# Kernel tuning notes

Measured on AMD Instinct MI355X. Metric: run time of the kernel, lower is better.

## Reference

```python
import jax, jax.numpy as jnp
import numpy as np

N_NODES = 100_000
N_EDGES = 3_200_000
F_IN = 64
HID = 16
N_CLASSES = 4


def setup_inputs() -> dict:
    key = jax.random.key(0)
    ks = jax.random.split(key, 9)
    x = jax.random.normal(ks[0], (N_NODES, F_IN), dtype=jnp.float32)
    edge_index = jax.random.randint(ks[1], (2, N_EDGES), 0, N_NODES, dtype=jnp.int64)
    edge_weight = jax.random.uniform(ks[2], (N_EDGES,), dtype=jnp.float32)
    # Glorot-style init for the three GCN layer weights, zero bias (PyG default)
    W1 = jax.random.normal(ks[3], (F_IN, HID), dtype=jnp.float32) * (1.0 / np.sqrt(F_IN))
    b1 = jnp.zeros((HID,), jnp.float32)
    W3 = jax.random.normal(ks[4], (HID, HID), dtype=jnp.float32) * (1.0 / np.sqrt(HID))
    b3 = jnp.zeros((HID,), jnp.float32)
    W2 = jax.random.normal(ks[5], (HID, N_CLASSES), dtype=jnp.float32) * (1.0 / np.sqrt(HID))
    b2 = jnp.zeros((N_CLASSES,), jnp.float32)
    return {"x": x, "edge_index": edge_index, "edge_weight": edge_weight,
            "W1": W1, "b1": b1, "W3": W3, "b3": b3, "W2": W2, "b2": b2}


def reference(x, edge_index, edge_weight, W1, b1, W3, b3, W2, b2):
    n = x.shape[0]
    # GCNConv default: add self-loops with weight 1, symmetric deg^-1/2 norm
    loop = jnp.arange(n, dtype=edge_index.dtype)
    row = jnp.concatenate([edge_index[0], loop])  # source nodes
    col = jnp.concatenate([edge_index[1], loop])  # target nodes
    ew = jnp.concatenate([edge_weight, jnp.ones((n,), edge_weight.dtype)])
    deg = jax.ops.segment_sum(ew, col, num_segments=n)
    dinv = jnp.where(deg > 0, jax.lax.rsqrt(deg), 0.0)
    norm = dinv[row] * ew * dinv[col]  # [E+N]

    def gcn_conv(h, W, b):
        h = h @ W                                  # [N, out] small matmul first
        msg = norm[:, None] * h[row]               # gather + scale, [E+N, out]
        return jax.ops.segment_sum(msg, col, num_segments=n) + b

    h = jax.nn.relu(gcn_conv(x, W1, b1))
    # dropout is identity in eval mode (training=False)
    h = jax.nn.relu(gcn_conv(h, W3, b3))
    h = gcn_conv(h, W2, b2)
    return jax.nn.log_softmax(h, axis=1)
```

## Files before the change

kernel.cpp:

```cpp
#include <hip/hip_runtime.h>
#include <math.h>

#define NN 100000
#define NE 3200000
#define F_IN 64
#define HID 16
#define NC 4

#define SZB 200
#define NB 500
#define CAP 7424
#define CH 8192
#define NCH 391
#define NW 16

typedef _Float16 half_t;
typedef _Float16 h4f __attribute__((ext_vector_type(4)));

__device__ __forceinline__ unsigned bdiv(unsigned c) {
    return (unsigned)(((unsigned long long)c * 167773ull) >> 25);
}

__device__ __forceinline__ float upw(int pk) {
    unsigned short us = (unsigned short)(pk & 0x7fff);
    half_t h;
    __builtin_memcpy(&h, &us, 2);
    return (float)h;
}

__global__ __launch_bounds__(1024) void k_bin(const int* __restrict__ row,
                                              const int* __restrict__ col,
                                              const float* __restrict__ ew,
                                              int* __restrict__ cursor,
                                              unsigned* __restrict__ bpk,
                                              unsigned char* __restrict__ bcl) {
    __shared__ int h[NB];
    __shared__ int lstart[NB];
    __shared__ int gbase[NB];
    __shared__ int wsum[8];
    __shared__ unsigned spk[CH];
    __shared__ unsigned short sbk[CH];
    __shared__ unsigned char scl[CH];
    int tid = threadIdx.x;
    int lane = tid & 63, wv = tid >> 6;
    for (int i = tid; i < NB; i += 1024) h[i] = 0;
    __syncthreads();
    int e0 = blockIdx.x * CH;
    int e1 = min(e0 + CH, NE);
    int eCnt = e1 - e0;
    for (int i = e0 + tid * 4; i < e1; i += 1024 * 4) {
        int4 c4 = *(const int4*)(col + i);
        atomicAdd(&h[bdiv(c4.x)], 1);
        atomicAdd(&h[bdiv(c4.y)], 1);
        atomicAdd(&h[bdiv(c4.z)], 1);
        atomicAdd(&h[bdiv(c4.w)], 1);
    }
    __syncthreads();
    int c0 = (tid < NB) ? h[tid] : 0;
    int v = c0;
#pragma unroll
    for (int off = 1; off < 64; off <<= 1) {
        int t = __shfl_up(v, off, 64);
        if (lane >= off) v += t;
    }
    if (wv < 8 && lane == 63) wsum[wv] = v;
    __syncthreads();
    if (tid < NB) {
        int pre = 0;
#pragma unroll
        for (int ww = 0; ww < 8; ww++) pre += (ww < wv) ? wsum[ww] : 0;
        int ex = (v + pre) - c0;
        lstart[tid] = ex;
        h[tid] = ex;
        if (c0) gbase[tid] = tid * CAP + atomicAdd(&cursor[tid], c0);
    }
    __syncthreads();
    for (int i = e0 + tid * 4; i < e1; i += 1024 * 4) {
        int4 c4 = *(const int4*)(col + i);
        int4 r4 = *(const int4*)(row + i);
        float4 w4 = *(const float4*)(ew + i);
        half_t hw0 = (half_t)w4.x, hw1 = (half_t)w4.y, hw2 = (half_t)w4.z, hw3 = (half_t)w4.w;
        unsigned short b0, b1, b2, b3;
        __builtin_memcpy(&b0, &hw0, 2); __builtin_memcpy(&b1, &hw1, 2);
        __builtin_memcpy(&b2, &hw2, 2); __builtin_memcpy(&b3, &hw3, 2);
        int p; unsigned bb;
        bb = bdiv(c4.x); p = atomicAdd(&h[bb], 1);
        spk[p] = ((unsigned)r4.x << 15) | (b0 & 0x7fff); scl[p] = (unsigned char)(c4.x - 200u * bb);
        sbk[p] = (unsigned short)bb;
        bb = bdiv(c4.y); p = atomicAdd(&h[bb], 1);
        spk[p] = ((unsigned)r4.y << 15) | (b1 & 0x7fff); scl[p] = (unsigned char)(c4.y - 200u * bb);
        sbk[p] = (unsigned short)bb;
        bb = bdiv(c4.z); p = atomicAdd(&h[bb], 1);
        spk[p] = ((unsigned)r4.z << 15) | (b2 & 0x7fff); scl[p] = (unsigned char)(c4.z - 200u * bb);
        sbk[p] = (unsigned short)bb;
        bb = bdiv(c4.w); p = atomicAdd(&h[bb], 1);
        spk[p] = ((unsigned)r4.w << 15) | (b3 & 0x7fff); scl[p] = (unsigned char)(c4.w - 200u * bb);
        sbk[p] = (unsigned short)bb;
    }
    __syncthreads();
    for (int i = tid; i < eCnt; i += 1024) {
        int lo = sbk[i];
        int d = gbase[lo] + (i - lstart[lo]);
        if (d < (lo + 1) * CAP) {
            bpk[d] = spk[i];
            bcl[d] = scl[i];
        }
    }
}

__global__ __launch_bounds__(1024) void k_sort(const unsigned* __restrict__ bpk,
                                               const unsigned char* __restrict__ bcl,
                                               const int* __restrict__ cursor,
                                               const float* __restrict__ x,
                                               const float* __restrict__ W1,
                                               unsigned* __restrict__ epk,
                                               int2* __restrict__ nodeptr2,
                                               float* __restrict__ dinv,
                                               half_t* __restrict__ tt1) {
    __shared__ int hw[NW][SZB];
    __shared__ int cnt[SZB];
    __shared__ int ps[SZB];
    __shared__ int wsum4[4];
    __shared__ unsigned stage[CAP];
    __shared__ float Ws[F_IN * HID];
    int b = blockIdx.x, tid = threadIdx.x;
    int lane = tid & 63;
    int w = tid >> 6;
    for (int i = tid; i < NW * SZB; i += 1024) ((int*)hw)[i] = 0;
    for (int i = tid; i < F_IN * HID; i += 1024) Ws[i] = W1[i];
    __syncthreads();
    int s = b * CAP;
    int m = min(cursor[b], CAP);
    int e = s + m;
    for (int i = s + tid; i < e; i += 1024)
        atomicAdd(&hw[w][bcl[i]], 1);
    __syncthreads();
    if (tid < SZB) {
        int c = 0;
#pragma unroll
        for (int ww = 0; ww < NW; ww++) c += hw[ww][tid];
        cnt[tid] = c;
    }
    __syncthreads();
    int pc = (tid < SZB) ? ((cnt[tid] + 3) & ~3) : 0;
    int v = pc;
#pragma unroll
    for (int off = 1; off < 64; off <<= 1) {
        int t = __shfl_up(v, off, 64);
        if (lane >= off) v += t;
    }
    if (w < 4 && lane == 63) wsum4[w] = v;
    __syncthreads();
    if (tid < SZB) {
        int pre = 0;
#pragma unroll
        for (int ww = 0; ww < 4; ww++) pre += (ww < w) ? wsum4[ww] : 0;
        ps[tid] = v + pre;
    }
    __syncthreads();
    if (tid < SZB) {
        int run = ps[tid] - pc;
#pragma unroll
        for (int ww = 0; ww < NW; ww++) {
            int t = hw[ww][tid];
            hw[ww][tid] = run;
            run += t;
        }
    }
    __syncthreads();
    int mpad = min(ps[SZB - 1], CAP);
    for (int i = tid; i < mpad; i += 1024) stage[i] = 0u;
    __syncthreads();
    for (int i = s + tid; i < e; i += 1024) {
        int cl = bcl[i];
        int pos = atomicAdd(&hw[w][cl], 1);
        if (pos < CAP) stage[pos] = bpk[i];
    }
    __syncthreads();
    for (int i = tid; i < mpad; i += 1024) epk[s + i] = stage[i];
    int nl = tid >> 2, l = tid & 3;
    float di = 0.0f;
    int n = b * SZB + nl;
    if (nl < SZB) {
        int pcn = (cnt[nl] + 3) & ~3;
        int ex = ps[nl] - pcn;
        float sw = 0.0f;
        for (int i = ex + l; i < ex + pcn; i += 4) sw += upw((int)stage[i]);
        sw += __shfl_xor(sw, 1, 4);
        sw += __shfl_xor(sw, 2, 4);
        di = rsqrtf(1.0f + sw);
        if (n < NN && l == 0) {
            nodeptr2[n] = make_int2(s + ex, s + ex + pcn);
            dinv[n] = di;
        }
    }
    if (nl < SZB && n < NN) {
        float part[HID];
#pragma unroll
        for (int j = 0; j < HID; j++) part[j] = 0.0f;
        const float4* xp = (const float4*)(x + (size_t)n * F_IN) + l * 4;
#pragma unroll
        for (int k4 = 0; k4 < 4; k4++) {
            float4 vx = xp[k4];
            int k = l * 16 + k4 * 4;
#pragma unroll
            for (int j = 0; j < HID; j++) {
                part[j] += vx.x * Ws[(k + 0) * HID + j];
                part[j] += vx.y * Ws[(k + 1) * HID + j];
                part[j] += vx.z * Ws[(k + 2) * HID + j];
                part[j] += vx.w * Ws[(k + 3) * HID + j];
            }
        }
#pragma unroll
        for (int j = 0; j < HID; j++) {
            part[j] += __shfl_xor(part[j], 1, 4);
            part[j] += __shfl_xor(part[j], 2, 4);
        }
        h4f o;
        o.x = (half_t)(di * part[4 * l + 0]);
        o.y = (half_t)(di * part[4 * l + 1]);
        o.z = (half_t)(di * part[4 * l + 2]);
        o.w = (half_t)(di * part[4 * l + 3]);
        ((h4f*)tt1)[n * 4 + l] = o;
    }
}

#define ACC4(Q, V0, V1, V2, V3)                                                 \
    do {                                                                        \
        float w0 = upw((Q).x), w1 = upw((Q).y), w2 = upw((Q).z), w3 = upw((Q).w); \
        ax += w0 * (float)(V0).x; ay += w0 * (float)(V0).y;                     \
        az += w0 * (float)(V0).z; aw += w0 * (float)(V0).w;                     \
        ax += w1 * (float)(V1).x; ay += w1 * (float)(V1).y;                     \
        az += w1 * (float)(V1).z; aw += w1 * (float)(V1).w;                     \
        ax += w2 * (float)(V2).x; ay += w2 * (float)(V2).y;                     \
        az += w2 * (float)(V2).z; aw += w2 * (float)(V2).w;                     \
        ax += w3 * (float)(V3).x; ay += w3 * (float)(V3).y;                     \
        az += w3 * (float)(V3).z; aw += w3 * (float)(V3).w;                     \
    } while (0)

template <int DN>
__global__ __launch_bounds__(256) void k_aggf(const unsigned* __restrict__ epk,
                                              const int2* __restrict__ nptr,
                                              const half_t* __restrict__ tt_in,
                                              const float* __restrict__ bias,
                                              const float* __restrict__ dinv,
                                              const float* __restrict__ Wn,
                                              half_t* __restrict__ tt_out) {
    __shared__ float Ws[HID * DN];
    if (threadIdx.x < HID * DN) Ws[threadIdx.x] = Wn[threadIdx.x];
    __syncthreads();
    int tid = blockIdx.x * 256 + threadIdx.x;
    int n = tid >> 2;
    int l = tid & 3;
    if (n >= NN) return;
    int2 p = nptr[n];
    const h4f* ttp = (const h4f*)tt_in;
    h4f sv = ttp[n * 4 + l];
    float ax = 0.f, ay = 0.f, az = 0.f, aw = 0.f;
    int base = p.x;
    const int pend = p.y;
    if (base < pend) {
        int4 q = *(const int4*)(epk + base);
        base += 4;
        bool more = base < pend;
        int4 qn = *(const int4*)(epk + (more ? base : p.x));
        h4f v0 = ttp[((((unsigned)q.x) >> 15) << 2) + l];
        h4f v1 = ttp[((((unsigned)q.y) >> 15) << 2) + l];
        h4f v2 = ttp[((((unsigned)q.z) >> 15) << 2) + l];
        h4f v3 = ttp[((((unsigned)q.w) >> 15) << 2) + l];
        while (more) {
            base += 4;
            bool more2 = base < pend;
            int4 qnn = *(const int4*)(epk + (more2 ? base : p.x));
            h4f u0 = ttp[((((unsigned)qn.x) >> 15) << 2) + l];
            h4f u1 = ttp[((((unsigned)qn.y) >> 15) << 2) + l];
            h4f u2 = ttp[((((unsigned)qn.z) >> 15) << 2) + l];
            h4f u3 = ttp[((((unsigned)qn.w) >> 15) << 2) + l];
            ACC4(q, v0, v1, v2, v3);
            q = qn; qn = qnn;
            v0 = u0; v1 = u1; v2 = u2; v3 = u3;
            more = more2;
        }
        ACC4(q, v0, v1, v2, v3);
    }
    float di = dinv[n];
    const float4* b4p = (const float4*)bias;
    float4 b4 = b4p[l];
    float hreg[4];
    hreg[0] = fmaxf(b4.x + di * (ax + (float)sv.x), 0.f);
    hreg[1] = fmaxf(b4.y + di * (ay + (float)sv.y), 0.f);
    hreg[2] = fmaxf(b4.z + di * (az + (float)sv.z), 0.f);
    hreg[3] = fmaxf(b4.w + di * (aw + (float)sv.w), 0.f);
    if (DN == 16) {
        float ox = 0.f, oy = 0.f, oz = 0.f, ow = 0.f;
#pragma unroll
        for (int k = 0; k < HID; k++) {
            float hk = __shfl(hreg[k & 3], k >> 2, 4);
            const float4 wk = *(const float4*)&Ws[k * 16 + 4 * l];
            ox += hk * wk.x; oy += hk * wk.y; oz += hk * wk.z; ow += hk * wk.w;
        }
        h4f ov;
        ov.x = (half_t)(di * ox); ov.y = (half_t)(di * oy);
        ov.z = (half_t)(di * oz); ov.w = (half_t)(di * ow);
        ((h4f*)tt_out)[n * 4 + l] = ov;
    } else {
        float o = 0.f;
#pragma unroll
        for (int k = 0; k < HID; k++) {
            float hk = __shfl(hreg[k & 3], k >> 2, 4);
            o += hk * Ws[k * DN + l];
        }
        tt_out[(size_t)n * DN + l] = (half_t)(di * o);
    }
}

__global__ __launch_bounds__(256) void k_agg4sm(const unsigned* __restrict__ epk,
                                                const int2* __restrict__ nptr,
                                                const half_t* __restrict__ tt,
                                                const float* __restrict__ bias,
                                                const float* __restrict__ dinv,
                                                float* __restrict__ out) {
    int tid = blockIdx.x * 256 + threadIdx.x;
    int n = tid >> 2;
    int l = tid & 3;
    if (n >= NN) return;
    int2 p = nptr[n];
    float self = (float)tt[n * 4 + l];
    float acc = 0.f;
    int base = p.x;
    const int pend = p.y;
    if (base < pend) {
        int4 q = *(const int4*)(epk + base);
        base += 4;
        bool more = base < pend;
        int4 qn = *(const int4*)(epk + (more ? base : p.x));
        float v0 = (float)tt[((((unsigned)q.x) >> 15) << 2) + l];
        float v1 = (float)tt[((((unsigned)q.y) >> 15) << 2) + l];
        float v2 = (float)tt[((((unsigned)q.z) >> 15) << 2) + l];
        float v3 = (float)tt[((((unsigned)q.w) >> 15) << 2) + l];
        while (more) {
            base += 4;
            bool more2 = base < pend;
            int4 qnn = *(const int4*)(epk + (more2 ? base : p.x));
            float u0 = (float)tt[((((unsigned)qn.x) >> 15) << 2) + l];
            float u1 = (float)tt[((((unsigned)qn.y) >> 15) << 2) + l];
            float u2 = (float)tt[((((unsigned)qn.z) >> 15) << 2) + l];
            float u3 = (float)tt[((((unsigned)qn.w) >> 15) << 2) + l];
            acc += upw(q.x) * v0;
            acc += upw(q.y) * v1;
            acc += upw(q.z) * v2;
            acc += upw(q.w) * v3;
            q = qn; qn = qnn;
            v0 = u0; v1 = u1; v2 = u2; v3 = u3;
            more = more2;
        }
        acc += upw(q.x) * v0;
        acc += upw(q.y) * v1;
        acc += upw(q.z) * v2;
        acc += upw(q.w) * v3;
    }
    float di = dinv[n];
    float logit = bias[l] + di * (acc + self);
    float mx = logit;
    mx = fmaxf(mx, __shfl_xor(mx, 1, 4));
    mx = fmaxf(mx, __shfl_xor(mx, 2, 4));
    float ex = expf(logit - mx);
    float sm = ex;
    sm += __shfl_xor(sm, 1, 4);
    sm += __shfl_xor(sm, 2, 4);
    out[n * 4 + l] = logit - mx - logf(sm);
}

extern "C" void kernel_launch(void* const* d_in, const int* in_sizes, int n_in,
                              void* d_out, int out_size, void* d_ws, size_t ws_size,
                              hipStream_t stream) {
    const float* x  = (const float*)d_in[0];
    const int*   ei = (const int*)d_in[1];
    const float* ew = (const float*)d_in[2];
    const float* W1 = (const float*)d_in[3];
    const float* b1 = (const float*)d_in[4];
    const float* W3 = (const float*)d_in[5];
    const float* b3 = (const float*)d_in[6];
    const float* W2 = (const float*)d_in[7];
    const float* b2 = (const float*)d_in[8];
    float* out = (float*)d_out;

    const int* row = ei;
    const int* col = ei + NE;

    const size_t NEP = (size_t)NB * CAP;
    char* ws = (char*)d_ws;
    size_t off = 0;
    float*         dinv     = (float*)(ws + off);         off += 400000;
    int2*          nodeptr2 = (int2*)(ws + off);          off += 800000;
    int*           cursor   = (int*)(ws + off);           off += 2048;
    unsigned*      epk      = (unsigned*)(ws + off);      off += NEP * 4;
    unsigned*      bpk      = (unsigned*)(ws + off);      off += NEP * 4;
    unsigned char* bcl      = (unsigned char*)(ws + off); off += (NEP + 15) & ~15ull;
    half_t*        tt1      = (half_t*)(ws + off);        off += (size_t)NN * HID * 2;
    half_t*        tt2      = (half_t*)(ws + off);        off += (size_t)NN * HID * 2;
    half_t*        tt3      = (half_t*)(ws + off);        off += (size_t)NN * NC * 2;

    hipMemsetAsync(cursor, 0, NB * sizeof(int), stream);

    k_bin<<<NCH, 1024, 0, stream>>>(row, col, ew, cursor, bpk, bcl);
    k_sort<<<NB, 1024, 0, stream>>>(bpk, bcl, cursor, x, W1, epk, nodeptr2, dinv, tt1);

    int gA = (NN * 4 + 255) / 256;

    k_aggf<HID><<<gA, 256, 0, stream>>>(epk, nodeptr2, tt1, b1, dinv, W3, tt2);
    k_aggf<NC><<<gA, 256, 0, stream>>>(epk, nodeptr2, tt2, b3, dinv, W2, tt3);
    k_agg4sm<<<gA, 256, 0, stream>>>(epk, nodeptr2, tt3, b2, dinv, out);
}
```

Before: 220.9 us.

## Use nontemporal loads/stores for streaming data and halve bin chunk size

Streaming reads and writes of edge lists, node pointers, features and outputs are switched to nontemporal loads and stores, so they pollute the cache less and leave room for the randomly gathered feature tables. The binning kernel now processes chunks of 4096 edges with 512-thread blocks, giving twice as many blocks with less shared memory each. The risk is that nontemporal hints hurt data that is reused soon, such as bpk/bcl, which are read again by the next kernel, and epk, which is re-read by all three aggregation passes.

```diff
diff --git a/kernel.cpp b/kernel.cpp
--- a/kernel.cpp
+++ b/kernel.cpp
@@ -10,12 +10,15 @@
 #define SZB 200
 #define NB 500
 #define CAP 7424
-#define CH 8192
-#define NCH 391
+#define CH 4096
+#define NCH 782
 #define NW 16
 
 typedef _Float16 half_t;
 typedef _Float16 h4f __attribute__((ext_vector_type(4)));
+typedef int i4v __attribute__((ext_vector_type(4)));
+typedef int i2v __attribute__((ext_vector_type(2)));
+typedef float f4v __attribute__((ext_vector_type(4)));
 
 __device__ __forceinline__ unsigned bdiv(unsigned c) {
     return (unsigned)(((unsigned long long)c * 167773ull) >> 25);
@@ -28,12 +31,12 @@
     return (float)h;
 }
 
-__global__ __launch_bounds__(1024) void k_bin(const int* __restrict__ row,
-                                              const int* __restrict__ col,
-                                              const float* __restrict__ ew,
-                                              int* __restrict__ cursor,
-                                              unsigned* __restrict__ bpk,
-                                              unsigned char* __restrict__ bcl) {
+__global__ __launch_bounds__(512) void k_bin(const int* __restrict__ row,
+                                             const int* __restrict__ col,
+                                             const float* __restrict__ ew,
+                                             int* __restrict__ cursor,
+                                             unsigned* __restrict__ bpk,
+                                             unsigned char* __restrict__ bcl) {
     __shared__ int h[NB];
     __shared__ int lstart[NB];
     __shared__ int gbase[NB];
@@ -43,12 +46,12 @@
     __shared__ unsigned char scl[CH];
     int tid = threadIdx.x;
     int lane = tid & 63, wv = tid >> 6;
-    for (int i = tid; i < NB; i += 1024) h[i] = 0;
+    for (int i = tid; i < NB; i += 512) h[i] = 0;
     __syncthreads();
     int e0 = blockIdx.x * CH;
     int e1 = min(e0 + CH, NE);
     int eCnt = e1 - e0;
-    for (int i = e0 + tid * 4; i < e1; i += 1024 * 4) {
+    for (int i = e0 + tid * 4; i < e1; i += 512 * 4) {
         int4 c4 = *(const int4*)(col + i);
         atomicAdd(&h[bdiv(c4.x)], 1);
         atomicAdd(&h[bdiv(c4.y)], 1);
@@ -63,7 +66,7 @@
         int t = __shfl_up(v, off, 64);
         if (lane >= off) v += t;
     }
-    if (wv < 8 && lane == 63) wsum[wv] = v;
+    if (lane == 63) wsum[wv] = v;
     __syncthreads();
     if (tid < NB) {
         int pre = 0;
@@ -75,10 +78,10 @@
         if (c0) gbase[tid] = tid * CAP + atomicAdd(&cursor[tid], c0);
     }
     __syncthreads();
-    for (int i = e0 + tid * 4; i < e1; i += 1024 * 4) {
+    for (int i = e0 + tid * 4; i < e1; i += 512 * 4) {
         int4 c4 = *(const int4*)(col + i);
-        int4 r4 = *(const int4*)(row + i);
-        float4 w4 = *(const float4*)(ew + i);
+        i4v r4 = __builtin_nontemporal_load((const i4v*)(row + i));
+        f4v w4 = __builtin_nontemporal_load((const f4v*)(ew + i));
         half_t hw0 = (half_t)w4.x, hw1 = (half_t)w4.y, hw2 = (half_t)w4.z, hw3 = (half_t)w4.w;
         unsigned short b0, b1, b2, b3;
         __builtin_memcpy(&b0, &hw0, 2); __builtin_memcpy(&b1, &hw1, 2);
@@ -98,12 +101,12 @@
         sbk[p] = (unsigned short)bb;
     }
     __syncthreads();
-    for (int i = tid; i < eCnt; i += 1024) {
+    for (int i = tid; i < eCnt; i += 512) {
         int lo = sbk[i];
         int d = gbase[lo] + (i - lstart[lo]);
         if (d < (lo + 1) * CAP) {
-            bpk[d] = spk[i];
-            bcl[d] = scl[i];
+            __builtin_nontemporal_store(spk[i], bpk + d);
+            __builtin_nontemporal_store(scl[i], bcl + d);
         }
     }
 }
@@ -172,12 +175,14 @@
     for (int i = tid; i < mpad; i += 1024) stage[i] = 0u;
     __syncthreads();
     for (int i = s + tid; i < e; i += 1024) {
-        int cl = bcl[i];
+        int cl = __builtin_nontemporal_load(bcl + i);
         int pos = atomicAdd(&hw[w][cl], 1);
-        if (pos < CAP) stage[pos] = bpk[i];
-    }
-    __syncthreads();
-    for (int i = tid; i < mpad; i += 1024) epk[s + i] = stage[i];
+        unsigned pk = __builtin_nontemporal_load(bpk + i);
+        if (pos < CAP) stage[pos] = pk;
+    }
+    __syncthreads();
+    for (int i = tid; i < mpad; i += 1024)
+        __builtin_nontemporal_store(stage[i], epk + s + i);
     int nl = tid >> 2, l = tid & 3;
     float di = 0.0f;
     int n = b * SZB + nl;
@@ -198,10 +203,10 @@
         float part[HID];
 #pragma unroll
         for (int j = 0; j < HID; j++) part[j] = 0.0f;
-        const float4* xp = (const float4*)(x + (size_t)n * F_IN) + l * 4;
+        const f4v* xp = (const f4v*)(x + (size_t)n * F_IN) + l * 4;
 #pragma unroll
         for (int k4 = 0; k4 < 4; k4++) {
-            float4 vx = xp[k4];
+            f4v vx = __builtin_nontemporal_load(xp + k4);
             int k = l * 16 + k4 * 4;
 #pragma unroll
             for (int j = 0; j < HID; j++) {
@@ -221,7 +226,7 @@
         o.y = (half_t)(di * part[4 * l + 1]);
         o.z = (half_t)(di * part[4 * l + 2]);
         o.w = (half_t)(di * part[4 * l + 3]);
-        ((h4f*)tt1)[n * 4 + l] = o;
+        __builtin_nontemporal_store(o, ((h4f*)tt1) + n * 4 + l);
     }
 }
 
@@ -253,17 +258,17 @@
     int n = tid >> 2;
     int l = tid & 3;
     if (n >= NN) return;
-    int2 p = nptr[n];
+    i2v p = __builtin_nontemporal_load((const i2v*)nptr + n);
     const h4f* ttp = (const h4f*)tt_in;
     h4f sv = ttp[n * 4 + l];
     float ax = 0.f, ay = 0.f, az = 0.f, aw = 0.f;
     int base = p.x;
     const int pend = p.y;
     if (base < pend) {
-        int4 q = *(const int4*)(epk + base);
+        i4v q = __builtin_nontemporal_load((const i4v*)(epk + base));
         base += 4;
         bool more = base < pend;
-        int4 qn = *(const int4*)(epk + (more ? base : p.x));
+        i4v qn = __builtin_nontemporal_load((const i4v*)(epk + (more ? base : p.x)));
         h4f v0 = ttp[((((unsigned)q.x) >> 15) << 2) + l];
         h4f v1 = ttp[((((unsigned)q.y) >> 15) << 2) + l];
         h4f v2 = ttp[((((unsigned)q.z) >> 15) << 2) + l];
@@ -271,7 +276,7 @@
         while (more) {
             base += 4;
             bool more2 = base < pend;
-            int4 qnn = *(const int4*)(epk + (more2 ? base : p.x));
+            i4v qnn = __builtin_nontemporal_load((const i4v*)(epk + (more2 ? base : p.x)));
             h4f u0 = ttp[((((unsigned)qn.x) >> 15) << 2) + l];
             h4f u1 = ttp[((((unsigned)qn.y) >> 15) << 2) + l];
             h4f u2 = ttp[((((unsigned)qn.z) >> 15) << 2) + l];
@@ -283,7 +288,7 @@
         }
         ACC4(q, v0, v1, v2, v3);
     }
-    float di = dinv[n];
+    float di = __builtin_nontemporal_load(dinv + n);
     const float4* b4p = (const float4*)bias;
     float4 b4 = b4p[l];
     float hreg[4];
@@ -302,7 +307,7 @@
         h4f ov;
         ov.x = (half_t)(di * ox); ov.y = (half_t)(di * oy);
         ov.z = (half_t)(di * oz); ov.w = (half_t)(di * ow);
-        ((h4f*)tt_out)[n * 4 + l] = ov;
+        __builtin_nontemporal_store(ov, ((h4f*)tt_out) + n * 4 + l);
     } else {
         float o = 0.f;
 #pragma unroll
@@ -310,7 +315,7 @@
             float hk = __shfl(hreg[k & 3], k >> 2, 4);
             o += hk * Ws[k * DN + l];
         }
-        tt_out[(size_t)n * DN + l] = (half_t)(di * o);
+        __builtin_nontemporal_store((half_t)(di * o), tt_out + (size_t)n * DN + l);
     }
 }
 
@@ -324,16 +329,16 @@
     int n = tid >> 2;
     int l = tid & 3;
     if (n >= NN) return;
-    int2 p = nptr[n];
+    i2v p = __builtin_nontemporal_load((const i2v*)nptr + n);
     float self = (float)tt[n * 4 + l];
     float acc = 0.f;
     int base = p.x;
     const int pend = p.y;
     if (base < pend) {
-        int4 q = *(const int4*)(epk + base);
+        i4v q = __builtin_nontemporal_load((const i4v*)(epk + base));
         base += 4;
         bool more = base < pend;
-        int4 qn = *(const int4*)(epk + (more ? base : p.x));
+        i4v qn = __builtin_nontemporal_load((const i4v*)(epk + (more ? base : p.x)));
         float v0 = (float)tt[((((unsigned)q.x) >> 15) << 2) + l];
         float v1 = (float)tt[((((unsigned)q.y) >> 15) << 2) + l];
         float v2 = (float)tt[((((unsigned)q.z) >> 15) << 2) + l];
@@ -341,7 +346,7 @@
         while (more) {
             base += 4;
             bool more2 = base < pend;
-            int4 qnn = *(const int4*)(epk + (more2 ? base : p.x));
+            i4v qnn = __builtin_nontemporal_load((const i4v*)(epk + (more2 ? base : p.x)));
             float u0 = (float)tt[((((unsigned)qn.x) >> 15) << 2) + l];
             float u1 = (float)tt[((((unsigned)qn.y) >> 15) << 2) + l];
             float u2 = (float)tt[((((unsigned)qn.z) >> 15) << 2) + l];
@@ -359,7 +364,7 @@
         acc += upw(q.z) * v2;
         acc += upw(q.w) * v3;
     }
-    float di = dinv[n];
+    float di = __builtin_nontemporal_load(dinv + n);
     float logit = bias[l] + di * (acc + self);
     float mx = logit;
     mx = fmaxf(mx, __shfl_xor(mx, 1, 4));
@@ -368,7 +373,7 @@
     float sm = ex;
     sm += __shfl_xor(sm, 1, 4);
     sm += __shfl_xor(sm, 2, 4);
-    out[n * 4 + l] = logit - mx - logf(sm);
+    __builtin_nontemporal_store(logit - mx - logf(sm), out + n * 4 + l);
 }
 
 extern "C" void kernel_launch(void* const* d_in, const int* in_sizes, int n_in,
@@ -403,7 +408,7 @@
 
     hipMemsetAsync(cursor, 0, NB * sizeof(int), stream);
 
-    k_bin<<<NCH, 1024, 0, stream>>>(row, col, ew, cursor, bpk, bcl);
+    k_bin<<<NCH, 512, 0, stream>>>(row, col, ew, cursor, bpk, bcl);
     k_sort<<<NB, 1024, 0, stream>>>(bpk, bcl, cursor, x, W1, epk, nodeptr2, dinv, tt1);
 
     int gA = (NN * 4 + 255) / 256;
```

Result: slower. 299.5 us (+35.5%).

## Degree-sort nodes per bucket for balanced aggregation; pack bin staging into uint2

Applied to the files above, without the earlier changes.

In k_sort, each bucket's 200 nodes are counting-sorted by padded degree into a perm array. The three aggregation kernels then index nodes through perm, so lanes within a wavefront get similar edge counts and lose less time to divergence. k_bin now packs its shared staging into one uint2 per edge and keeps the col loads in registers instead of reading them twice. This adds an indirection load per node, scatters the output writes, and extra work in k_sort.

```diff
diff --git a/kernel.cpp b/kernel.cpp
--- a/kernel.cpp
+++ b/kernel.cpp
@@ -37,10 +37,8 @@
     __shared__ int h[NB];
     __shared__ int lstart[NB];
     __shared__ int gbase[NB];
-    __shared__ int wsum[8];
-    __shared__ unsigned spk[CH];
-    __shared__ unsigned short sbk[CH];
-    __shared__ unsigned char scl[CH];
+    __shared__ int wsum[16];
+    __shared__ uint2 s2[CH];
     int tid = threadIdx.x;
     int lane = tid & 63, wv = tid >> 6;
     for (int i = tid; i < NB; i += 1024) h[i] = 0;
@@ -48,12 +46,18 @@
     int e0 = blockIdx.x * CH;
     int e1 = min(e0 + CH, NE);
     int eCnt = e1 - e0;
-    for (int i = e0 + tid * 4; i < e1; i += 1024 * 4) {
-        int4 c4 = *(const int4*)(col + i);
-        atomicAdd(&h[bdiv(c4.x)], 1);
-        atomicAdd(&h[bdiv(c4.y)], 1);
-        atomicAdd(&h[bdiv(c4.z)], 1);
-        atomicAdd(&h[bdiv(c4.w)], 1);
+    int4 c4s[2];
+#pragma unroll
+    for (int it = 0; it < 2; it++) {
+        int i = e0 + tid * 4 + it * 4096;
+        if (i < e1) {
+            int4 c4 = *(const int4*)(col + i);
+            c4s[it] = c4;
+            atomicAdd(&h[bdiv(c4.x)], 1);
+            atomicAdd(&h[bdiv(c4.y)], 1);
+            atomicAdd(&h[bdiv(c4.z)], 1);
+            atomicAdd(&h[bdiv(c4.w)], 1);
+        }
     }
     __syncthreads();
     int c0 = (tid < NB) ? h[tid] : 0;
@@ -63,7 +67,7 @@
         int t = __shfl_up(v, off, 64);
         if (lane >= off) v += t;
     }
-    if (wv < 8 && lane == 63) wsum[wv] = v;
+    if (lane == 63) wsum[wv] = v;
     __syncthreads();
     if (tid < NB) {
         int pre = 0;
@@ -75,35 +79,40 @@
         if (c0) gbase[tid] = tid * CAP + atomicAdd(&cursor[tid], c0);
     }
     __syncthreads();
-    for (int i = e0 + tid * 4; i < e1; i += 1024 * 4) {
-        int4 c4 = *(const int4*)(col + i);
-        int4 r4 = *(const int4*)(row + i);
-        float4 w4 = *(const float4*)(ew + i);
-        half_t hw0 = (half_t)w4.x, hw1 = (half_t)w4.y, hw2 = (half_t)w4.z, hw3 = (half_t)w4.w;
-        unsigned short b0, b1, b2, b3;
-        __builtin_memcpy(&b0, &hw0, 2); __builtin_memcpy(&b1, &hw1, 2);
-        __builtin_memcpy(&b2, &hw2, 2); __builtin_memcpy(&b3, &hw3, 2);
-        int p; unsigned bb;
-        bb = bdiv(c4.x); p = atomicAdd(&h[bb], 1);
-        spk[p] = ((unsigned)r4.x << 15) | (b0 & 0x7fff); scl[p] = (unsigned char)(c4.x - 200u * bb);
-        sbk[p] = (unsigned short)bb;
-        bb = bdiv(c4.y); p = atomicAdd(&h[bb], 1);
-        spk[p] = ((unsigned)r4.y << 15) | (b1 & 0x7fff); scl[p] = (unsigned char)(c4.y - 200u * bb);
-        sbk[p] = (unsigned short)bb;
-        bb = bdiv(c4.z); p = atomicAdd(&h[bb], 1);
-        spk[p] = ((unsigned)r4.z << 15) | (b2 & 0x7fff); scl[p] = (unsigned char)(c4.z - 200u * bb);
-        sbk[p] = (unsigned short)bb;
-        bb = bdiv(c4.w); p = atomicAdd(&h[bb], 1);
-        spk[p] = ((unsigned)r4.w << 15) | (b3 & 0x7fff); scl[p] = (unsigned char)(c4.w - 200u * bb);
-        sbk[p] = (unsigned short)bb;
+#pragma unroll
+    for (int it = 0; it < 2; it++) {
+        int i = e0 + tid * 4 + it * 4096;
+        if (i < e1) {
+            int4 c4 = c4s[it];
+            int4 r4 = *(const int4*)(row + i);
+            float4 w4 = *(const float4*)(ew + i);
+            half_t hw0 = (half_t)w4.x, hw1 = (half_t)w4.y, hw2 = (half_t)w4.z, hw3 = (half_t)w4.w;
+            unsigned short b0, b1, b2, b3;
+            __builtin_memcpy(&b0, &hw0, 2); __builtin_memcpy(&b1, &hw1, 2);
+            __builtin_memcpy(&b2, &hw2, 2); __builtin_memcpy(&b3, &hw3, 2);
+            int p; unsigned bb;
+            bb = bdiv(c4.x); p = atomicAdd(&h[bb], 1);
+            s2[p] = make_uint2(((unsigned)r4.x << 15) | (b0 & 0x7fff),
+                               (bb << 8) | (unsigned)(c4.x - 200u * bb));
+            bb = bdiv(c4.y); p = atomicAdd(&h[bb], 1);
+            s2[p] = make_uint2(((unsigned)r4.y << 15) | (b1 & 0x7fff),
+                               (bb << 8) | (unsigned)(c4.y - 200u * bb));
+            bb = bdiv(c4.z); p = atomicAdd(&h[bb], 1);
+            s2[p] = make_uint2(((unsigned)r4.z << 15) | (b2 & 0x7fff),
+                               (bb << 8) | (unsigned)(c4.z - 200u * bb));
+            bb = bdiv(c4.w); p = atomicAdd(&h[bb], 1);
+            s2[p] = make_uint2(((unsigned)r4.w << 15) | (b3 & 0x7fff),
+                               (bb << 8) | (unsigned)(c4.w - 200u * bb));
+        }
     }
     __syncthreads();
     for (int i = tid; i < eCnt; i += 1024) {
-        int lo = sbk[i];
+        uint2 e2 = s2[i];
+        int lo = (int)(e2.y >> 8);
         int d = gbase[lo] + (i - lstart[lo]);
         if (d < (lo + 1) * CAP) {
-            bpk[d] = spk[i];
-            bcl[d] = scl[i];
+            bpk[d] = e2.x;
+            bcl[d] = (unsigned char)(e2.y & 255u);
         }
     }
 }
@@ -116,11 +125,14 @@
                                                unsigned* __restrict__ epk,
                                                int2* __restrict__ nodeptr2,
                                                float* __restrict__ dinv,
-                                               half_t* __restrict__ tt1) {
+                                               half_t* __restrict__ tt1,
+                                               int* __restrict__ perm) {
     __shared__ int hw[NW][SZB];
     __shared__ int cnt[SZB];
     __shared__ int ps[SZB];
     __shared__ int wsum4[4];
+    __shared__ int h2[64];
+    __shared__ int h2b[64];
     __shared__ unsigned stage[CAP];
     __shared__ float Ws[F_IN * HID];
     int b = blockIdx.x, tid = threadIdx.x;
@@ -128,6 +140,7 @@
     int w = tid >> 6;
     for (int i = tid; i < NW * SZB; i += 1024) ((int*)hw)[i] = 0;
     for (int i = tid; i < F_IN * HID; i += 1024) Ws[i] = W1[i];
+    if (tid < 64) h2[tid] = 0;
     __syncthreads();
     int s = b * CAP;
     int m = min(cursor[b], CAP);
@@ -143,6 +156,11 @@
     }
     __syncthreads();
     int pc = (tid < SZB) ? ((cnt[tid] + 3) & ~3) : 0;
+    int key = 0;
+    if (tid < SZB) {
+        key = min(pc >> 2, 63);
+        atomicAdd(&h2[key], 1);
+    }
     int v = pc;
 #pragma unroll
     for (int off = 1; off < 64; off <<= 1) {
@@ -157,7 +175,21 @@
         for (int ww = 0; ww < 4; ww++) pre += (ww < w) ? wsum4[ww] : 0;
         ps[tid] = v + pre;
     }
-    __syncthreads();
+    if (tid < 64) {
+        int c2 = h2[tid];
+        int v2 = c2;
+#pragma unroll
+        for (int off = 1; off < 64; off <<= 1) {
+            int t = __shfl_up(v2, off, 64);
+            if (lane >= off) v2 += t;
+        }
+        h2b[tid] = v2 - c2;
+    }
+    __syncthreads();
+    if (tid < SZB) {
+        int rk = atomicAdd(&h2b[key], 1);
+        perm[b * SZB + rk] = b * SZB + tid;
+    }
     if (tid < SZB) {
         int run = ps[tid] - pc;
 #pragma unroll
@@ -241,6 +273,7 @@
 template <int DN>
 __global__ __launch_bounds__(256) void k_aggf(const unsigned* __restrict__ epk,
                                               const int2* __restrict__ nptr,
+                                              const int* __restrict__ perm,
                                               const half_t* __restrict__ tt_in,
                                               const float* __restrict__ bias,
                                               const float* __restrict__ dinv,
@@ -250,9 +283,10 @@
     if (threadIdx.x < HID * DN) Ws[threadIdx.x] = Wn[threadIdx.x];
     __syncthreads();
     int tid = blockIdx.x * 256 + threadIdx.x;
-    int n = tid >> 2;
+    int g = tid >> 2;
     int l = tid & 3;
-    if (n >= NN) return;
+    if (g >= NN) return;
+    int n = perm[g];
     int2 p = nptr[n];
     const h4f* ttp = (const h4f*)tt_in;
     h4f sv = ttp[n * 4 + l];
@@ -316,14 +350,16 @@
 
 __global__ __launch_bounds__(256) void k_agg4sm(const unsigned* __restrict__ epk,
                                                 const int2* __restrict__ nptr,
+                                                const int* __restrict__ perm,
                                                 const half_t* __restrict__ tt,
                                                 const float* __restrict__ bias,
                                                 const float* __restrict__ dinv,
                                                 float* __restrict__ out) {
     int tid = blockIdx.x * 256 + threadIdx.x;
-    int n = tid >> 2;
+    int g = tid >> 2;
     int l = tid & 3;
-    if (n >= NN) return;
+    if (g >= NN) return;
+    int n = perm[g];
     int2 p = nptr[n];
     float self = (float)tt[n * 4 + l];
     float acc = 0.f;
@@ -394,6 +430,7 @@
     float*         dinv     = (float*)(ws + off);         off += 400000;
     int2*          nodeptr2 = (int2*)(ws + off);          off += 800000;
     int*           cursor   = (int*)(ws + off);           off += 2048;
+    int*           perm     = (int*)(ws + off);           off += 400000;
     unsigned*      epk      = (unsigned*)(ws + off);      off += NEP * 4;
     unsigned*      bpk      = (unsigned*)(ws + off);      off += NEP * 4;
     unsigned char* bcl      = (unsigned char*)(ws + off); off += (NEP + 15) & ~15ull;
@@ -404,11 +441,11 @@
     hipMemsetAsync(cursor, 0, NB * sizeof(int), stream);
 
     k_bin<<<NCH, 1024, 0, stream>>>(row, col, ew, cursor, bpk, bcl);
-    k_sort<<<NB, 1024, 0, stream>>>(bpk, bcl, cursor, x, W1, epk, nodeptr2, dinv, tt1);
+    k_sort<<<NB, 1024, 0, stream>>>(bpk, bcl, cursor, x, W1, epk, nodeptr2, dinv, tt1, perm);
 
     int gA = (NN * 4 + 255) / 256;
 
-    k_aggf<HID><<<gA, 256, 0, stream>>>(epk, nodeptr2, tt1, b1, dinv, W3, tt2);
-    k_aggf<NC><<<gA, 256, 0, stream>>>(epk, nodeptr2, tt2, b3, dinv, W2, tt3);
-    k_agg4sm<<<gA, 256, 0, stream>>>(epk, nodeptr2, tt3, b2, dinv, out);
-}
+    k_aggf<HID><<<gA, 256, 0, stream>>>(epk, nodeptr2, perm, tt1, b1, dinv, W3, tt2);
+    k_aggf<NC><<<gA, 256, 0, stream>>>(epk, nodeptr2, perm, tt2, b3, dinv, W2, tt3);
+    k_agg4sm<<<gA, 256, 0, stream>>>(epk, nodeptr2, perm, tt3, b2, dinv, out);
+}
```

New measurement: 223.7 us. Within noise of the previous version (+1.3%).
